# Optimization experiments

Measured on AMD Instinct MI355X. Metric: run time of the kernel, lower is better.

The kernel has to match this reference:

```python
import jax, jax.numpy as jnp
import numpy as np

HEAD, DIM, R = 8, 256, 3
RA = (2 * R + 1) ** 2  # 49


def conv2d(x, w, b=None, pad=0, groups=1):
    y = jax.lax.conv_general_dilated(x, w, (1, 1), [(pad, pad), (pad, pad)],
                                     dimension_numbers=('NCHW', 'OIHW', 'NCHW'),
                                     feature_group_count=groups)
    return y if b is None else y + b[None, :, None, None]


def grid_sample(img, grid, mode, padding='zeros'):
    # img [B,C,H,W]; grid [B,Hg,Wg,2] with (x,y) in [-1,1]; align_corners=False.
    B, C, H, W = img.shape
    Hg, Wg = grid.shape[1], grid.shape[2]
    gx = ((grid[..., 0] + 1.0) * W - 1.0) / 2.0
    gy = ((grid[..., 1] + 1.0) * H - 1.0) / 2.0
    if padding == 'border':
        gx = jnp.clip(gx, 0.0, W - 1.0)
        gy = jnp.clip(gy, 0.0, H - 1.0)
    gx = gx.reshape(B, -1)
    gy = gy.reshape(B, -1)

    def gather(iy, ix):
        iyc = jnp.clip(iy, 0, H - 1)
        ixc = jnp.clip(ix, 0, W - 1)
        return jax.vmap(lambda im, a, b: im[:, a, b])(img, iyc, ixc)  # [B,C,N]

    def mask(iy, ix):
        if padding == 'border':
            return jnp.ones(iy.shape, img.dtype)
        return ((ix >= 0) & (ix < W) & (iy >= 0) & (iy < H)).astype(img.dtype)

    if mode == 'nearest':
        ix = jnp.round(gx).astype(jnp.int32)
        iy = jnp.round(gy).astype(jnp.int32)
        out = gather(iy, ix) * mask(iy, ix)[:, None, :]
    else:  # bilinear
        x0f = jnp.floor(gx); y0f = jnp.floor(gy)
        wx = gx - x0f; wy = gy - y0f
        x0 = x0f.astype(jnp.int32); y0 = y0f.astype(jnp.int32)
        out = jnp.zeros((B, C, gx.shape[1]), img.dtype)
        for dx, dy, w in ((0, 0, (1 - wx) * (1 - wy)), (1, 0, wx * (1 - wy)),
                          (0, 1, (1 - wx) * wy), (1, 1, wx * wy)):
            ix = x0 + dx; iy = y0 + dy
            out = out + gather(iy, ix) * (w * mask(iy, ix))[:, None, :]
    return out.reshape(B, C, Hg, Wg)


def mlp2(x, W1, b1, W2, b2):
    return jax.nn.relu(x @ W1.T + b1) @ W2.T + b2


def setup_inputs() -> dict:
    key = jax.random.key(0)
    ks = jax.random.split(key, 32)
    B, H, W, Q = 1, 64, 64, 4096
    f32 = jnp.float32
    rn = lambda k, shp, s=0.02: jax.random.normal(k, shp, f32) * s
    return {
        'inp': jax.random.normal(ks[0], (B, 3, H, W), f32),
        'coord': jax.random.uniform(ks[1], (B, Q, 2), f32, -1.0, 1.0),
        'cell': jnp.full((B, Q, 2), 2.0 / (2 * H), f32),
        'W_enc': rn(ks[2], (64, 3, 3, 3)), 'b_enc': jnp.zeros((64,), f32),
        'W_ch': rn(ks[3], (256, 64, 3, 3)), 'b_ch': jnp.zeros((256,), f32),
        'W_q': rn(ks[4], (256, 256, 3, 3)), 'b_q': jnp.zeros((256,), f32),
        'W_k': rn(ks[5], (256, 256, 3, 3)), 'b_k': jnp.zeros((256,), f32),
        'W_v': rn(ks[6], (256, 256, 3, 3)), 'b_v': jnp.zeros((256,), f32),
        'W_off1': rn(ks[7], (256, 32, 5, 5)), 'b_off1': jnp.zeros((256,), f32),
        'ln_g': jnp.ones((256,), f32), 'ln_b': jnp.zeros((256,), f32),
        'W_off2': rn(ks[8], (98, 256, 1, 1)),
        'Wc1': rn(ks[9], (256, 98)), 'bc1': jnp.zeros((256,), f32),
        'Wc2': rn(ks[10], (49, 256)), 'bc2': jnp.zeros((49,), f32),
        'Wi1': rn(ks[11], (256, 12546)), 'bi1': jnp.zeros((256,), f32),
        'Wi2': rn(ks[12], (3, 256)), 'bi2': jnp.zeros((3,), f32),
        'scale': 2,
    }


def reference(inp, coord, cell, W_enc, b_enc, W_ch, b_ch, W_q, b_q, W_k, b_k,
              W_v, b_v, W_off1, b_off1, ln_g, ln_b, W_off2, Wc1, bc1, Wc2, bc2,
              Wi1, bi1, Wi2, bi2, scale):
    B, _, H, W = inp.shape
    Q = coord.shape[1]
    # gen_feat: encoder stub (conv+relu) -> conv_ch -> q/k/v convs
    feat = conv2d(jax.nn.relu(conv2d(inp, W_enc, b_enc, pad=1)), W_ch, b_ch, pad=1)
    fq = conv2d(feat, W_q, b_q, pad=1)
    fk = conv2d(feat, W_k, b_k, pad=1)
    fv = conv2d(feat, W_v, b_v, pad=1)
    # offset branch: grouped 5x5 conv -> channelwise LN -> GELU -> 1x1 conv (no bias)
    o = conv2d(feat, W_off1, b_off1, pad=2, groups=8)
    oc = o.transpose(0, 2, 3, 1)
    mu = oc.mean(-1, keepdims=True)
    var = ((oc - mu) ** 2).mean(-1, keepdims=True)
    oc = (oc - mu) / jnp.sqrt(var + 1e-5) * ln_g + ln_b
    offsets = conv2d(jax.nn.gelu(oc.transpose(0, 3, 1, 2), approximate=False), W_off2, None, pad=0)  # [B,98,H,W]
    # LR coordinate grid (y,x) at pixel centers in [-1,1]
    ys = -1.0 + 1.0 / H + (2.0 / H) * jnp.arange(H, dtype=inp.dtype)
    xs = -1.0 + 1.0 / W + (2.0 / W) * jnp.arange(W, dtype=inp.dtype)
    coord_lr = jnp.broadcast_to(jnp.stack(jnp.meshgrid(ys, xs, indexing='ij'), 0)[None], (B, 2, H, W))
    sc = coord[:, :, None, :]          # [B,Q,1,2] (y,x)
    g = sc[..., ::-1]                  # (x,y) for grid_sample
    sck = grid_sample(coord_lr, g, 'nearest').transpose(0, 2, 3, 1)  # [B,Q,1,2]
    off = grid_sample(offsets, g, 'nearest').transpose(0, 2, 3, 1).reshape(B, Q, RA, 2)
    off = jnp.tanh(off) * jnp.array([1.0 / (H - 1.0), 1.0 / (W - 1.0)], inp.dtype) * 2.0
    d = jnp.linspace(-R, R, 2 * R + 1).astype(inp.dtype)
    delta = jnp.stack(jnp.meshgrid(d * (2.0 / H), d * (2.0 / W), indexing='ij'), -1).reshape(1, 1, RA, 2)
    sck = sck + delta + off            # [B,Q,49,2] sampling locs (y,x)
    q = grid_sample(fq, g, 'bilinear').transpose(0, 2, 3, 1).reshape(B, Q, HEAD, DIM // HEAD)
    k = grid_sample(fk, sck[..., ::-1], 'nearest').transpose(0, 2, 3, 1).reshape(B, Q, RA, HEAD, DIM // HEAD)
    v = grid_sample(fv, sck[..., ::-1], 'nearest').transpose(0, 2, 3, 1).reshape(B, Q, RA, HEAD, DIM // HEAD)
    attn_val = jnp.einsum('bqhd,bqkhd->bqkh', q, k) / np.sqrt(DIM // HEAD)  # [B,Q,49,8]
    rel = (sc - sck) * jnp.array([H, W], inp.dtype)  # [B,Q,49,2]
    wcoord = mlp2(rel.reshape(B * Q, RA * 2), Wc1, bc1, Wc2, bc2).reshape(B, Q, RA, 1)
    attn = jax.nn.softmax(wcoord + attn_val, axis=2)  # softmax over 49 samples
    feat_in = (v * attn[..., None]).reshape(B, Q, RA * DIM)
    rel_cell = cell * jnp.array([H, W], inp.dtype)
    feat_in = jnp.concatenate([feat_in, rel_cell], -1)  # [B,Q,12546]
    pred = mlp2(feat_in.reshape(B * Q, -1), Wi1, bi1, Wi2, bi2).reshape(B, Q, 3)
    skip = grid_sample(inp, g, 'bilinear', 'border')[:, :, :, 0].transpose(0, 2, 1)
    return pred + skip
```

## Files before the change

### kernel.cpp

```cpp
#include <hip/hip_runtime.h>
#include <hip/hip_bf16.h>


typedef unsigned short u16;
typedef unsigned int u32;
using frag_ab = __attribute__((ext_vector_type(8))) short;
using frag_cd = __attribute__((ext_vector_type(4))) float;

#define HW 4096
#define NQ 4096
#define KBIG 12576
#define SPLITK 16
#define KCHUNK 800
#define KQ 2304
#define QSPLIT 2
#define QCHUNK 1152

static __device__ __forceinline__ u16 f2b(float f) {
  union { __hip_bfloat16 h; u16 u; } c; c.h = __float2bfloat16(f); return c.u;
}
static __device__ __forceinline__ float b2f(u16 v) {
  return __uint_as_float((u32)v << 16);
}
static __device__ __forceinline__ u32 pk2(float a, float b) {
  union { __hip_bfloat162 h; u32 u; } c;
  c.h = __float22bfloat162_rn(float2{a, b});
  return c.u;
}
static __device__ __forceinline__ void glds16(const u16* g, u16* l) {
  __builtin_amdgcn_global_load_lds(
      (const __attribute__((address_space(1))) u32*)(g),
      (__attribute__((address_space(3))) u32*)(l), 16, 0, 0);
}

#define BM 64
#define BN 64
#define BK 32
#define LDSS 40

__global__ __launch_bounds__(256)
void gemm_bt(const u16* __restrict__ A, const u16* __restrict__ Bt,
             void* __restrict__ Cv, const float* __restrict__ bias,
             int N, int K, int ldc, int flags,
             long sA, long sB, long sC, int sBias)
{
  __shared__ u16 As[BM * LDSS];
  __shared__ u16 Bs[BN * LDSS];
  const int z = blockIdx.z;
  A  += (long)z * sA;
  Bt += (long)z * sB;
  const float* bz = bias ? bias + (long)z * sBias : nullptr;

  const int tid  = threadIdx.x;
  const int m0   = blockIdx.x * BM;
  const int n0   = blockIdx.y * BN;
  const int wave = tid >> 6, lane = tid & 63;
  const int mw = (wave & 1) * 32, nw = (wave >> 1) * 32;
  const int lr = lane & 15, lk = lane >> 4;
  const int srow = tid >> 2, scol = (tid & 3) * 8;

  frag_cd acc[2][2] = {};
  const u16* aptr = A + (size_t)(m0 + srow) * K + scol;
  const bool bok  = (n0 + srow) < N;
  const u16* bptr = Bt + (size_t)(n0 + srow) * K + scol;

  uint4 av = *(const uint4*)(aptr);
  uint4 bv = bok ? *(const uint4*)(bptr) : uint4{0u, 0u, 0u, 0u};

  for (int k0 = 0; k0 < K; k0 += BK) {
    *(uint4*)&As[srow * LDSS + scol] = av;
    *(uint4*)&Bs[srow * LDSS + scol] = bv;
    __syncthreads();
    if (k0 + BK < K) {
      av = *(const uint4*)(aptr + k0 + BK);
      bv = bok ? *(const uint4*)(bptr + k0 + BK) : uint4{0u, 0u, 0u, 0u};
    }
    frag_ab af0 = *(const frag_ab*)&As[(mw      + lr) * LDSS + lk * 8];
    frag_ab af1 = *(const frag_ab*)&As[(mw + 16 + lr) * LDSS + lk * 8];
    frag_ab bf0 = *(const frag_ab*)&Bs[(nw      + lr) * LDSS + lk * 8];
    frag_ab bf1 = *(const frag_ab*)&Bs[(nw + 16 + lr) * LDSS + lk * 8];
    acc[0][0] = __builtin_amdgcn_mfma_f32_16x16x32_bf16(af0, bf0, acc[0][0], 0, 0, 0);
    acc[0][1] = __builtin_amdgcn_mfma_f32_16x16x32_bf16(af0, bf1, acc[0][1], 0, 0, 0);
    acc[1][0] = __builtin_amdgcn_mfma_f32_16x16x32_bf16(af1, bf0, acc[1][0], 0, 0, 0);
    acc[1][1] = __builtin_amdgcn_mfma_f32_16x16x32_bf16(af1, bf1, acc[1][1], 0, 0, 0);
    __syncthreads();
  }

  const bool relu = flags & 1;
  const bool obf  = flags & 2;
  #pragma unroll
  for (int i = 0; i < 2; i++)
    #pragma unroll
    for (int j = 0; j < 2; j++) {
      int col = n0 + nw + j * 16 + lr;
      if (col >= N) continue;
      float badd = bz ? bz[col] : 0.f;
      #pragma unroll
      for (int r = 0; r < 4; r++) {
        int row = m0 + mw + i * 16 + lk * 4 + r;
        float v = acc[i][j][r] + badd;
        if (relu) v = fmaxf(v, 0.f);
        size_t idx = (size_t)z * sC + (size_t)row * ldc + col;
        if (obf) ((u16*)Cv)[idx] = f2b(v);
        else     ((float*)Cv)[idx] = v;
      }
    }
}

template<int W3, int SH, int PAD>
__global__ __launch_bounds__(256)
void gemm_conv(const u16* __restrict__ feat, const u16* __restrict__ Bt,
               void* __restrict__ Cv, const float* __restrict__ bias,
               int N, int K, int ldc, int flags, int FC, int cbStride,
               long sB, long sC, int sBias)
{
  __shared__ u16 As[BM * LDSS];
  __shared__ u16 Bs[BN * LDSS];
  const int z = blockIdx.z;
  Bt += (long)z * sB;
  const float* bz = bias ? bias + (long)z * sBias : nullptr;
  const int cb = z * cbStride;

  const int tid  = threadIdx.x;
  const int m0   = blockIdx.x * BM;
  const int n0   = blockIdx.y * BN;
  const int wave = tid >> 6, lane = tid & 63;
  const int mw = (wave & 1) * 32, nw = (wave >> 1) * 32;
  const int lr = lane & 15, lk = lane >> 4;
  const int srow = tid >> 2, scol = (tid & 3) * 8;
  const int p = m0 + srow, y = p >> 6, x = p & 63;

  frag_cd acc[2][2] = {};
  const bool bok  = (n0 + srow) < N;
  const u16* bptr = Bt + (size_t)(n0 + srow) * K + scol;

  auto stageA = [&](int k0) -> uint4 {
    int k = k0 + scol;
    int s = k >> SH;
    int c = k & ((1 << SH) - 1);
    int dy = s / W3, dx = s - dy * W3;
    int yy = y + dy - PAD, xx = x + dx - PAD;
    if (((unsigned)yy < 64u) && ((unsigned)xx < 64u))
      return *(const uint4*)&feat[(size_t)(yy * 64 + xx) * FC + cb + c];
    return uint4{0u, 0u, 0u, 0u};
  };

  uint4 av = stageA(0);
  uint4 bv = bok ? *(const uint4*)(bptr) : uint4{0u, 0u, 0u, 0u};

  for (int k0 = 0; k0 < K; k0 += BK) {
    *(uint4*)&As[srow * LDSS + scol] = av;
    *(uint4*)&Bs[srow * LDSS + scol] = bv;
    __syncthreads();
    if (k0 + BK < K) {
      av = stageA(k0 + BK);
      bv = bok ? *(const uint4*)(bptr + k0 + BK) : uint4{0u, 0u, 0u, 0u};
    }
    frag_ab af0 = *(const frag_ab*)&As[(mw      + lr) * LDSS + lk * 8];
    frag_ab af1 = *(const frag_ab*)&As[(mw + 16 + lr) * LDSS + lk * 8];
    frag_ab bf0 = *(const frag_ab*)&Bs[(nw      + lr) * LDSS + lk * 8];
    frag_ab bf1 = *(const frag_ab*)&Bs[(nw + 16 + lr) * LDSS + lk * 8];
    acc[0][0] = __builtin_amdgcn_mfma_f32_16x16x32_bf16(af0, bf0, acc[0][0], 0, 0, 0);
    acc[0][1] = __builtin_amdgcn_mfma_f32_16x16x32_bf16(af0, bf1, acc[0][1], 0, 0, 0);
    acc[1][0] = __builtin_amdgcn_mfma_f32_16x16x32_bf16(af1, bf0, acc[1][0], 0, 0, 0);
    acc[1][1] = __builtin_amdgcn_mfma_f32_16x16x32_bf16(af1, bf1, acc[1][1], 0, 0, 0);
    __syncthreads();
  }

  const bool relu = flags & 1;
  const bool obf  = flags & 2;
  #pragma unroll
  for (int i = 0; i < 2; i++)
    #pragma unroll
    for (int j = 0; j < 2; j++) {
      int col = n0 + nw + j * 16 + lr;
      if (col >= N) continue;
      float badd = bz ? bz[col] : 0.f;
      #pragma unroll
      for (int r = 0; r < 4; r++) {
        int row = m0 + mw + i * 16 + lk * 4 + r;
        float v = acc[i][j][r] + badd;
        if (relu) v = fmaxf(v, 0.f);
        size_t idx = (size_t)z * sC + (size_t)row * ldc + col;
        if (obf) ((u16*)Cv)[idx] = f2b(v);
        else     ((float*)Cv)[idx] = v;
      }
    }
}

__global__ __launch_bounds__(256)
void gemm_qkv(const u16* __restrict__ feat, const u16* __restrict__ Bt,
              u16* __restrict__ P)
{
  __shared__ u16 As[64 * LDSS];
  __shared__ u16 Bs[128 * 32];
  const int tid  = threadIdx.x;
  const int m0   = blockIdx.x * 64;
  const int n0   = blockIdx.y * 128;
  const int z    = blockIdx.z;
  const int kbeg = z * QCHUNK;
  const int kend = kbeg + QCHUNK;
  const int wave = tid >> 6, lane = tid & 63;
  const int nw = wave * 32;
  const int lr = lane & 15, lk = lane >> 4;
  const int arow = tid >> 2, acol = (tid & 3) * 8;
  const int p = m0 + arow, y = p >> 6, x = p & 63;

  frag_cd acc[4][2] = {};
  const u16* bbase = Bt + (size_t)(n0 + (tid >> 2)) * KQ + (tid & 3) * 8 + kbeg;
  u16* bdst = &Bs[(size_t)tid * 8];

  auto stageA = [&](int k0) -> uint4 {
    int k = k0 + acol;
    int s = k >> 8, c = k & 255;
    int dy = s / 3, dx = s - dy * 3;
    int yy = y + dy - 1, xx = x + dx - 1;
    if (((unsigned)yy < 64u) && ((unsigned)xx < 64u))
      return *(const uint4*)&feat[(size_t)(yy * 64 + xx) * 256 + c];
    return uint4{0u, 0u, 0u, 0u};
  };

  uint4 av = stageA(kbeg);

  for (int k0 = kbeg; k0 < kend; k0 += BK) {
    glds16(bbase + (k0 - kbeg), bdst);
    glds16(bbase + (k0 - kbeg) + (size_t)64 * KQ, bdst + 2048);
    *(uint4*)&As[arow * LDSS + acol] = av;
    __syncthreads();
    if (k0 + BK < kend) av = stageA(k0 + BK);
    frag_ab af[4];
    #pragma unroll
    for (int i = 0; i < 4; i++)
      af[i] = *(const frag_ab*)&As[(i * 16 + lr) * LDSS + lk * 8];
    #pragma unroll
    for (int j = 0; j < 2; j++) {
      frag_ab bf = *(const frag_ab*)&Bs[(nw + j * 16 + lr) * 32 + lk * 8];
      #pragma unroll
      for (int i = 0; i < 4; i++)
        acc[i][j] = __builtin_amdgcn_mfma_f32_16x16x32_bf16(af[i], bf, acc[i][j], 0, 0, 0);
    }
    __syncthreads();
  }

  #pragma unroll
  for (int i = 0; i < 4; i++)
    #pragma unroll
    for (int j = 0; j < 2; j++) {
      int col = n0 + nw + j * 16 + lr;
      #pragma unroll
      for (int r = 0; r < 4; r++) {
        int row = m0 + i * 16 + lk * 4 + r;
        P[(size_t)z * (NQ * 768) + (size_t)row * 768 + col] = f2b(acc[i][j][r]);
      }
    }
}

__global__ __launch_bounds__(256)
void reduce_qkv(const u16* __restrict__ P, const float* __restrict__ bias,
                u16* __restrict__ outb, float* __restrict__ outV)
{
  int i8 = blockIdx.x * 256 + threadIdx.x;
  if (i8 >= NQ * 96) return;
  size_t i = (size_t)i8 * 8;
  int row = (int)(i / 768);
  int c = (int)(i % 768);
  uint4 a = *(const uint4*)&P[i];
  uint4 b = *(const uint4*)&P[(size_t)NQ * 768 + i];
  u32 aw[4] = {a.x, a.y, a.z, a.w};
  u32 bw[4] = {b.x, b.y, b.z, b.w};
  float v[8];
  #pragma unroll
  for (int t = 0; t < 4; t++) {
    v[2 * t]     = __uint_as_float(aw[t] << 16) + __uint_as_float(bw[t] << 16)
                 + bias[c + 2 * t];
    v[2 * t + 1] = __uint_as_float(aw[t] & 0xffff0000u)
                 + __uint_as_float(bw[t] & 0xffff0000u) + bias[c + 2 * t + 1];
  }
  uint4 ob = {pk2(v[0], v[1]), pk2(v[2], v[3]), pk2(v[4], v[5]), pk2(v[6], v[7])};
  *(uint4*)&outb[i] = ob;
  if (c >= 512) {
    float* dst = outV + (size_t)row * 256 + (c - 512);
    *(float4*)dst       = float4{v[0], v[1], v[2], v[3]};
    *(float4*)(dst + 4) = float4{v[4], v[5], v[6], v[7]};
  }
}

__global__ __launch_bounds__(512, 4)
void gemm_big(const u16* __restrict__ Bt, const float* __restrict__ fqkvV,
              const float* __restrict__ attnval, const int* __restrict__ vidx,
              const float* __restrict__ cell, u16* __restrict__ P)
{
  __shared__ u16 As[128 * LDSS];
  __shared__ u16 Bs[256 * 32];
  __shared__ int   s_vidx[5 * 128];
  __shared__ float s_attn[5 * 128 * 8];
  const int tid  = threadIdx.x;
  const int m0   = blockIdx.x * 128;
  const int z    = blockIdx.y;
  const int kbeg = z * KCHUNK;
  const int kend = min(KBIG, kbeg + KCHUNK);
  const int jbeg = kbeg >> 8;
  const int jcnt = ((kend - 1) >> 8) - jbeg + 1;
  const int wave = tid >> 6, lane = tid & 63;
  const int mw = (wave & 1) * 64, nwv = (wave >> 1) * 64;
  const int lr = lane & 15, lk = lane >> 4;
  const int arow = tid >> 2, acol = (tid & 3) * 8;
  const int q = m0 + arow;

  for (int t = tid; t < 128 * jcnt; t += 512) {
    int r = t & 127, jj = t >> 7;
    int j = jbeg + jj;
    s_vidx[t] = (j < 49) ? vidx[(m0 + r) * 49 + j] : -1;
  }
  for (int t = tid; t < 128 * 8 * jcnt; t += 512) {
    int h = t & 7, rr = (t >> 3) & 127, jj = t >> 10;
    int j = jbeg + jj;
    s_attn[t] = (j < 49) ? attnval[((size_t)((m0 + rr) * 49 + j)) * 8 + h] : 0.f;
  }
  __syncthreads();

  auto loadA = [&](int k0, float4& f0, float4& f1, float& w) {
    const int k = k0 + acol;
    const int j = k >> 8, c = k & 255;
    f0 = float4{0.f, 0.f, 0.f, 0.f};
    f1 = float4{0.f, 0.f, 0.f, 0.f};
    w = 0.f;
    if (j < 49) {
      const int jj = j - jbeg;
      int id = s_vidx[jj * 128 + arow];
      if (id >= 0) {
        w = s_attn[(jj * 128 + arow) * 8 + (c >> 5)];
        const float* src = fqkvV + (size_t)id * 256 + c;
        f0 = *(const float4*)src;
        f1 = *(const float4*)(src + 4);
      }
    } else if (c == 0) {
      f0.x = cell[q * 2]; f0.y = cell[q * 2 + 1];
      w = 64.f;
    }
  };

  frag_cd acc[4][4] = {};
  float4 f0c, f1c; float wc_;
  loadA(kbeg, f0c, f1c, wc_);
  const u16* bbase = Bt + (size_t)(tid >> 2) * KBIG + (tid & 3) * 8 + kbeg;
  u16* bdst = &Bs[(size_t)tid * 8];

  for (int k0 = kbeg; k0 < kend; k0 += BK) {
    glds16(bbase + (k0 - kbeg), bdst);
    glds16(bbase + (k0 - kbeg) + (size_t)128 * KBIG, bdst + 4096);
    {
      uint4 av;
      av.x = pk2(f0c.x * wc_, f0c.y * wc_);
      av.y = pk2(f0c.z * wc_, f0c.w * wc_);
      av.z = pk2(f1c.x * wc_, f1c.y * wc_);
      av.w = pk2(f1c.z * wc_, f1c.w * wc_);
      *(uint4*)&As[arow * LDSS + acol] = av;
    }
    __syncthreads();
    if (k0 + BK < kend) loadA(k0 + BK, f0c, f1c, wc_);
    frag_ab af[4];
    #pragma unroll
    for (int i = 0; i < 4; i++)
      af[i] = *(const frag_ab*)&As[(mw + i * 16 + lr) * LDSS + lk * 8];
    #pragma unroll
    for (int j = 0; j < 4; j++) {
      frag_ab bf = *(const frag_ab*)&Bs[(nwv + j * 16 + lr) * 32 + lk * 8];
      #pragma unroll
      for (int i = 0; i < 4; i++)
        acc[i][j] = __builtin_amdgcn_mfma_f32_16x16x32_bf16(af[i], bf, acc[i][j], 0, 0, 0);
    }
    __syncthreads();
  }

  #pragma unroll
  for (int i = 0; i < 4; i++)
    #pragma unroll
    for (int j = 0; j < 4; j++) {
      int col = nwv + j * 16 + lr;
      #pragma unroll
      for (int r = 0; r < 4; r++) {
        int row = m0 + mw + i * 16 + lk * 4 + r;
        P[(size_t)z * (NQ * 256) + (size_t)row * 256 + col] = f2b(acc[i][j][r]);
      }
    }
}

__global__ __launch_bounds__(256)
void reduce_final(const u16* __restrict__ Pb, const float* __restrict__ bi1,
                  const float* __restrict__ Wi2, const float* __restrict__ bi2,
                  const float* __restrict__ skipb, float* __restrict__ out)
{
  const int q = blockIdx.x, c = threadIdx.x;
  float s = 0.f;
  #pragma unroll
  for (int z = 0; z < SPLITK; z++)
    s += b2f(Pb[(size_t)z * (NQ * 256) + (size_t)q * 256 + c]);
  s += bi1[c];
  s = fmaxf(s, 0.f);

  __shared__ float part[3][4];
  float p0 = s * Wi2[c], p1 = s * Wi2[256 + c], p2 = s * Wi2[512 + c];
  #pragma unroll
  for (int off = 32; off; off >>= 1) {
    p0 += __shfl_xor(p0, off);
    p1 += __shfl_xor(p1, off);
    p2 += __shfl_xor(p2, off);
  }
  if ((c & 63) == 0) {
    int w = c >> 6;
    part[0][w] = p0; part[1][w] = p1; part[2][w] = p2;
  }
  __syncthreads();
  if (c < 3)
    out[q * 3 + c] = bi2[c] + skipb[q * 3 + c]
                   + part[c][0] + part[c][1] + part[c][2] + part[c][3];
}

static __device__ __forceinline__
void packconv(const float* __restrict__ W, u16* __restrict__ Bt,
              int Cin, int K2, int idx)
{
  int o  = idx / (Cin * K2);
  int r  = idx - o * (Cin * K2);
  int ci = r / K2;
  int s  = r - ci * K2;
  Bt[(size_t)o * (Cin * K2) + s * Cin + ci] = f2b(W[idx]);
}
static __device__ __forceinline__
void packcast(const float* __restrict__ W, u16* __restrict__ Bt,
              int Kin, int Kout, int idx)
{
  int n = idx / Kout, k = idx - n * Kout;
  Bt[idx] = f2b(k < Kin ? W[(size_t)n * Kin + k] : 0.f);
}

#define SZ_CH   147456
#define SZ_QKV  589824
#define SZ_OFF1 204800
#define SZ_OFF2 25088
#define SZ_C1   32768
#define SZ_C2   12544
#define SZ_PACK (SZ_CH + 3*SZ_QKV + SZ_OFF1 + SZ_OFF2 + SZ_C1 + SZ_C2 + 768)

__global__ void pack_misc(const float* W_ch, const float* W_q, const float* W_k,
                          const float* W_v, const float* W_off1, const float* W_off2,
                          const float* Wc1, const float* Wc2,
                          const float* b_q, const float* b_k, const float* b_v,
                          u16* Btch, u16* Btqkv, u16* Btoff1, u16* Btoff2,
                          u16* Btc1, u16* Btc2, float* bqkv)
{
  int i = blockIdx.x * 256 + threadIdx.x;
  if (i < SZ_CH) { packconv(W_ch, Btch, 64, 9, i); return; }
  i -= SZ_CH;
  if (i < SZ_QKV) { packconv(W_q, Btqkv, 256, 9, i); return; }
  i -= SZ_QKV;
  if (i < SZ_QKV) { packconv(W_k, Btqkv + (size_t)256 * 2304, 256, 9, i); return; }
  i -= SZ_QKV;
  if (i < SZ_QKV) { packconv(W_v, Btqkv + (size_t)512 * 2304, 256, 9, i); return; }
  i -= SZ_QKV;
  if (i < SZ_OFF1) { packconv(W_off1, Btoff1, 32, 25, i); return; }
  i -= SZ_OFF1;
  if (i < SZ_OFF2) { packcast(W_off2, Btoff2, 256, 256, i); return; }
  i -= SZ_OFF2;
  if (i < SZ_C1) { packcast(Wc1, Btc1, 98, 128, i); return; }
  i -= SZ_C1;
  if (i < SZ_C2) { packcast(Wc2, Btc2, 256, 256, i); return; }
  i -= SZ_C2;
  if (i < 768) {
    bqkv[i] = (i < 256) ? b_q[i] : (i < 512) ? b_k[i - 256] : b_v[i - 512];
  }
}

__global__ void pack_cast(const float* __restrict__ W, u16* __restrict__ Bt,
                          int N, int Kin, int Kout)
{
  int idx = blockIdx.x * 256 + threadIdx.x;
  if (idx >= N * Kout) return;
  int n = idx / Kout, k = idx - n * Kout;
  Bt[idx] = f2b(k < Kin ? W[(size_t)n * Kin + k] : 0.f);
}

__global__ __launch_bounds__(64)
void conv_enc(const float* __restrict__ inp, const float* __restrict__ W,
              const float* __restrict__ b, u16* __restrict__ feat1)
{
  const int p = blockIdx.x, c = threadIdx.x;
  const int y = p >> 6, x = p & 63;
  float s = b[c];
  #pragma unroll
  for (int ci = 0; ci < 3; ci++)
    #pragma unroll
    for (int dy = 0; dy < 3; dy++) {
      int yy = y + dy - 1;
      if ((unsigned)yy >= 64u) continue;
      #pragma unroll
      for (int dx = 0; dx < 3; dx++) {
        int xx = x + dx - 1;
        if ((unsigned)xx >= 64u) continue;
        s += inp[ci * HW + yy * 64 + xx] * W[((c * 3 + ci) * 3 + dy) * 3 + dx];
      }
    }
  feat1[(size_t)p * 64 + c] = f2b(fmaxf(s, 0.f));
}

__global__ __launch_bounds__(256)
void ln_gelu(const float* __restrict__ x, const float* __restrict__ g,
             const float* __restrict__ b, u16* __restrict__ y)
{
  const int p = blockIdx.x, c = threadIdx.x;
  __shared__ float r1[4], r2[4];
  float v = x[(size_t)p * 256 + c];
  float s1 = v, s2 = v * v;
  #pragma unroll
  for (int off = 32; off; off >>= 1) {
    s1 += __shfl_xor(s1, off);
    s2 += __shfl_xor(s2, off);
  }
  if ((c & 63) == 0) { r1[c >> 6] = s1; r2[c >> 6] = s2; }
  __syncthreads();
  float t1 = r1[0] + r1[1] + r1[2] + r1[3];
  float t2 = r2[0] + r2[1] + r2[2] + r2[3];
  float mu  = t1 * (1.f / 256.f);
  float var = t2 * (1.f / 256.f) - mu * mu;
  float xn = (v - mu) * rsqrtf(var + 1e-5f) * g[c] + b[c];
  float ge = 0.5f * xn * (1.f + erff(xn * 0.70710678118654752f));
  y[(size_t)p * 256 + c] = f2b(ge);
}

__global__ __launch_bounds__(256)
void sampler(const float* __restrict__ coord, const u16* __restrict__ fqkvb,
             const float* __restrict__ offs, const float* __restrict__ inp,
             float* __restrict__ attnval, u16* __restrict__ relbuf,
             int* __restrict__ vidx, float* __restrict__ skipb)
{
  const int q = blockIdx.x;
  const int tid = threadIdx.x;
  __shared__ float s_off[98];
  __shared__ int s_idx[49];
  __shared__ float s_q[256];

  const float c0 = coord[q * 2], c1 = coord[q * 2 + 1];
  const float gxp = ((c1 + 1.f) * 64.f - 1.f) * 0.5f;
  const float gyp = ((c0 + 1.f) * 64.f - 1.f) * 0.5f;
  const int ixn = (int)rintf(gxp), iyn = (int)rintf(gyp);
  const bool inn = ((unsigned)ixn < 64u) && ((unsigned)iyn < 64u);

  if (tid < 98) {
    float v = inn ? offs[(size_t)(iyn * 64 + ixn) * 98 + tid] : 0.f;
    s_off[tid] = tanhf(v) * (2.f / 63.f);
  }
  __syncthreads();

  const float scky = inn ? (-1.f + (float)(2 * iyn + 1) * (1.f / 64.f)) : 0.f;
  const float sckx = inn ? (-1.f + (float)(2 * ixn + 1) * (1.f / 64.f)) : 0.f;

  if (tid < 49) {
    const int a = tid / 7, bb = tid - a * 7;
    float sy = scky + (float)(a - 3) * (2.f / 64.f) + s_off[2 * tid];
    float sx = sckx + (float)(bb - 3) * (2.f / 64.f) + s_off[2 * tid + 1];
    relbuf[(size_t)q * 128 + 2 * tid]     = f2b((c0 - sy) * 64.f);
    relbuf[(size_t)q * 128 + 2 * tid + 1] = f2b((c1 - sx) * 64.f);
    float gx2 = ((sx + 1.f) * 64.f - 1.f) * 0.5f;
    float gy2 = ((sy + 1.f) * 64.f - 1.f) * 0.5f;
    int ix2 = (int)rintf(gx2), iy2 = (int)rintf(gy2);
    int id = (((unsigned)ix2 < 64u) && ((unsigned)iy2 < 64u)) ? (iy2 * 64 + ix2) : -1;
    s_idx[tid] = id;
    vidx[q * 49 + tid] = id;
  } else if (tid >= 98 && tid < 128) {
    relbuf[(size_t)q * 128 + tid] = 0;
  }

  {
    const float x0f = floorf(gxp), y0f = floorf(gyp);
    const float wx = gxp - x0f, wy = gyp - y0f;
    const int x0 = (int)x0f, y0 = (int)y0f;
    float qc = 0.f;
    #pragma unroll
    for (int t = 0; t < 4; t++) {
      int xi = x0 + (t & 1), yi = y0 + (t >> 1);
      if (((unsigned)xi < 64u) && ((unsigned)yi < 64u)) {
        float w = ((t & 1) ? wx : 1.f - wx) * ((t >> 1) ? wy : 1.f - wy);
        qc += w * b2f(fqkvb[(size_t)(yi * 64 + xi) * 768 + tid]);
      }
    }
    s_q[tid] = qc * 0.17677669529663687f;
  }

  if (tid < 3) {
    float gx = fminf(fmaxf(gxp, 0.f), 63.f);
    float gy = fminf(fmaxf(gyp, 0.f), 63.f);
    float xf = floorf(gx), yf = floorf(gy);
    float wxs = gx - xf, wys = gy - yf;
    int xa = (int)xf, ya = (int)yf;
    int xb = min(xa + 1, 63), yb = min(ya + 1, 63);
    const float* ch = inp + tid * HW;
    float v = (1.f - wxs) * (1.f - wys) * ch[ya * 64 + xa]
            + wxs * (1.f - wys) * ch[ya * 64 + xb]
            + (1.f - wxs) * wys * ch[yb * 64 + xa]
            + wxs * wys * ch[yb * 64 + xb];
    skipb[q * 3 + tid] = v;
  }
  __syncthreads();

  const int wave = tid >> 6, lane = tid & 63;
  const int half = lane >> 5, sub = lane & 31;
  const int ch0 = sub * 8;
  const int h = sub >> 2;
  float qv[8];
  #pragma unroll
  for (int i = 0; i < 8; i++) qv[i] = s_q[ch0 + i];

  for (int it = 0; it < 7; it++) {
    int j = it * 8 + wave * 2 + half;
    if (j >= 49) break;
    int id = s_idx[j];
    float p = 0.f;
    if (id >= 0) {
      uint4 kv = *(const uint4*)&fqkvb[(size_t)id * 768 + 256 + ch0];
      u32 w0 = kv.x, w1 = kv.y, w2 = kv.z, w3 = kv.w;
      p = fmaf(qv[0], __uint_as_float(w0 << 16), p);
      p = fmaf(qv[1], __uint_as_float(w0 & 0xffff0000u), p);
      p = fmaf(qv[2], __uint_as_float(w1 << 16), p);
      p = fmaf(qv[3], __uint_as_float(w1 & 0xffff0000u), p);
      p = fmaf(qv[4], __uint_as_float(w2 << 16), p);
      p = fmaf(qv[5], __uint_as_float(w2 & 0xffff0000u), p);
      p = fmaf(qv[6], __uint_as_float(w3 << 16), p);
      p = fmaf(qv[7], __uint_as_float(w3 & 0xffff0000u), p);
    }
    p += __shfl_down(p, 2, 4);
    p += __shfl_down(p, 1, 4);
    if ((sub & 3) == 0) attnval[((size_t)q * 49 + j) * 8 + h] = p;
  }
}

__global__ __launch_bounds__(512)
void softmax_k(const float* __restrict__ wc, float* __restrict__ attnval)
{
  const int q = blockIdx.x;
  const int tid = threadIdx.x;
  const int hh = tid >> 6, l = tid & 63;
  float v = (l < 49) ? wc[(size_t)q * 49 + l] + attnval[((size_t)q * 49 + l) * 8 + hh]
                     : -1e30f;
  float m = v;
  #pragma unroll
  for (int off = 32; off; off >>= 1) m = fmaxf(m, __shfl_xor(m, off));
  float e = (l < 49) ? expf(v - m) : 0.f;
  float s = e;
  #pragma unroll
  for (int off = 32; off; off >>= 1) s += __shfl_xor(s, off);
  if (l < 49) attnval[((size_t)q * 49 + l) * 8 + hh] = e / s;
}

extern "C" void kernel_launch(void* const* d_in, const int* in_sizes, int n_in,
                              void* d_out, int out_size, void* d_ws, size_t ws_size,
                              hipStream_t stream)
{
  const float* inp    = (const float*)d_in[0];
  const float* coord  = (const float*)d_in[1];
  const float* cell   = (const float*)d_in[2];
  const float* W_enc  = (const float*)d_in[3];
  const float* b_enc  = (const float*)d_in[4];
  const float* W_ch   = (const float*)d_in[5];
  const float* b_ch   = (const float*)d_in[6];
  const float* W_q    = (const float*)d_in[7];
  const float* b_q    = (const float*)d_in[8];
  const float* W_k    = (const float*)d_in[9];
  const float* b_k    = (const float*)d_in[10];
  const float* W_v    = (const float*)d_in[11];
  const float* b_v    = (const float*)d_in[12];
  const float* W_off1 = (const float*)d_in[13];
  const float* b_off1 = (const float*)d_in[14];
  const float* ln_g   = (const float*)d_in[15];
  const float* ln_b   = (const float*)d_in[16];
  const float* W_off2 = (const float*)d_in[17];
  const float* Wc1    = (const float*)d_in[18];
  const float* bc1    = (const float*)d_in[19];
  const float* Wc2    = (const float*)d_in[20];
  const float* bc2    = (const float*)d_in[21];
  const float* Wi1    = (const float*)d_in[22];
  const float* bi1    = (const float*)d_in[23];
  const float* Wi2    = (const float*)d_in[24];
  const float* bi2    = (const float*)d_in[25];

  char* base = (char*)d_ws;
  size_t off = 0;
  auto alloc = [&](size_t bytes) -> char* {
    char* r = base + off;
    off = (off + bytes + 255) & ~(size_t)255;
    return r;
  };

  float* obuf   = (float*)alloc((size_t)HW * 256 * 4);
  u16*   ocg    = (u16*)  alloc((size_t)HW * 256 * 2);
  float* offsb  = (float*)alloc((size_t)HW * 98 * 4);
  u16*   feat1  = (u16*)  alloc((size_t)HW * 64 * 2);
  u16*   feat   = (u16*)  alloc((size_t)HW * 256 * 2);
  u16*   hid1   = (u16*)  alloc((size_t)NQ * 256 * 2);
  float* wcb    = (float*)alloc((size_t)NQ * 49 * 4);
  u16*   relbuf = (u16*)  alloc((size_t)NQ * 128 * 2);
  u16*   Btqkv  = (u16*)  alloc((size_t)768 * 2304 * 2);
  u16*   Btch   = (u16*)  alloc((size_t)256 * 576 * 2);
  u16*   Btoff1 = (u16*)  alloc((size_t)256 * 800 * 2);
  u16*   Btoff2 = (u16*)  alloc((size_t)98 * 256 * 2);
  u16*   Btc1   = (u16*)  alloc((size_t)256 * 128 * 2);
  u16*   Btc2   = (u16*)  alloc((size_t)49 * 256 * 2);
  u16* Pb = (u16*)base;
  u16* Pqb = (u16*)(base + ((size_t)36 << 20));
  {
    size_t need = ((size_t)36 << 20) + (size_t)QSPLIT * NQ * 768 * 2;
    if (off < need) off = (need + 255) & ~(size_t)255;
  }
  u16*   fqkvb   = (u16*)  alloc((size_t)HW * 768 * 2);
  float* fqkvV   = (float*)alloc((size_t)HW * 256 * 4);
  float* attnval = (float*)alloc((size_t)NQ * 49 * 8 * 4);
  int*   vidxb   = (int*)  alloc((size_t)NQ * 49 * 4);
  float* skipb   = (float*)alloc((size_t)NQ * 3 * 4);
  u16*   Wi1p    = (u16*)  alloc((size_t)256 * KBIG * 2);
  float* bqkv    = (float*)alloc(768 * 4);
  (void)ws_size; (void)in_sizes; (void)n_in; (void)out_size;

  pack_misc<<<(SZ_PACK + 255) / 256, 256, 0, stream>>>(
      W_ch, W_q, W_k, W_v, W_off1, W_off2, Wc1, Wc2, b_q, b_k, b_v,
      Btch, Btqkv, Btoff1, Btoff2, Btc1, Btc2, bqkv);
  pack_cast<<<(256 * KBIG + 255) / 256, 256, 0, stream>>>(Wi1, Wi1p, 256, 12546, KBIG);

  conv_enc<<<HW, 64, 0, stream>>>(inp, W_enc, b_enc, feat1);
  gemm_conv<3, 6, 1><<<dim3(64, 4, 1), 256, 0, stream>>>(
      feat1, Btch, feat, b_ch, 256, 576, 256, 2, 64, 0, 0, 0, 0);
  gemm_qkv<<<dim3(64, 6, QSPLIT), 256, 0, stream>>>(feat, Btqkv, Pqb);
  reduce_qkv<<<(NQ * 96 + 255) / 256, 256, 0, stream>>>(Pqb, bqkv, fqkvb, fqkvV);
  gemm_conv<5, 5, 2><<<dim3(64, 1, 8), 256, 0, stream>>>(
      feat, Btoff1, obuf, b_off1, 32, 800, 256, 0, 256, 32,
      (long)32 * 800, 32, 32);
  ln_gelu<<<HW, 256, 0, stream>>>(obuf, ln_g, ln_b, ocg);
  gemm_bt<<<dim3(64, 2, 1), 256, 0, stream>>>(ocg, Btoff2, offsb, nullptr,
      98, 256, 98, 0, 0, 0, 0, 0);

  sampler<<<NQ, 256, 0, stream>>>(coord, fqkvb, offsb, inp,
                                  attnval, relbuf, vidxb, skipb);
  gemm_bt<<<dim3(64, 4, 1), 256, 0, stream>>>(relbuf, Btc1, hid1, bc1,
      256, 128, 256, 3, 0, 0, 0, 0);
  gemm_bt<<<dim3(64, 1, 1), 256, 0, stream>>>(hid1, Btc2, wcb, bc2,
      49, 256, 49, 0, 0, 0, 0, 0);
  softmax_k<<<NQ, 512, 0, stream>>>(wcb, attnval);

  gemm_big<<<dim3(32, SPLITK), 512, 0, stream>>>(
      Wi1p, fqkvV, attnval, vidxb, cell, Pb);
  reduce_final<<<NQ, 256, 0, stream>>>(Pb, bi1, Wi2, bi2, skipb, (float*)d_out);
}
```

Before: 293.9 us.

## Fuse coordinate MLP and softmax into one kernel, merge weight packing, split QKV three ways

Replaces the two small coordinate-MLP GEMM launches and the softmax kernel with a single coord_mlp kernel. It keeps the hidden layer in LDS, converts Wc2 to bf16 on the fly and applies softmax per query/head in place on attnval. This drops launches and global round trips, but runs only 64 blocks and uses a serial per-thread softmax over 49 strided global loads. The Wi1 cast is folded into the main pack kernel, and the QKV split-K goes from 2 to 3 with a generalized reduce.

New measurement: 326.9 us. 11.2% more time.

```diff
diff --git a/kernel.cpp b/kernel.cpp
--- a/kernel.cpp
+++ b/kernel.cpp
@@ -13,8 +13,8 @@
 #define SPLITK 16
 #define KCHUNK 800
 #define KQ 2304
-#define QSPLIT 2
-#define QCHUNK 1152
+#define QSPLIT 3
+#define QCHUNK 768
 
 static __device__ __forceinline__ u16 f2b(float f) {
   union { __hip_bfloat16 h; u16 u; } c; c.h = __float2bfloat16(f); return c.u;
@@ -264,17 +264,17 @@
   size_t i = (size_t)i8 * 8;
   int row = (int)(i / 768);
   int c = (int)(i % 768);
-  uint4 a = *(const uint4*)&P[i];
-  uint4 b = *(const uint4*)&P[(size_t)NQ * 768 + i];
-  u32 aw[4] = {a.x, a.y, a.z, a.w};
-  u32 bw[4] = {b.x, b.y, b.z, b.w};
   float v[8];
   #pragma unroll
-  for (int t = 0; t < 4; t++) {
-    v[2 * t]     = __uint_as_float(aw[t] << 16) + __uint_as_float(bw[t] << 16)
-                 + bias[c + 2 * t];
-    v[2 * t + 1] = __uint_as_float(aw[t] & 0xffff0000u)
-                 + __uint_as_float(bw[t] & 0xffff0000u) + bias[c + 2 * t + 1];
+  for (int t = 0; t < 8; t++) v[t] = bias[c + t];
+  for (int z = 0; z < QSPLIT; z++) {
+    uint4 a = *(const uint4*)&P[(size_t)z * (NQ * 768) + i];
+    u32 aw[4] = {a.x, a.y, a.z, a.w};
+    #pragma unroll
+    for (int t = 0; t < 4; t++) {
+      v[2 * t]     += __uint_as_float(aw[t] << 16);
+      v[2 * t + 1] += __uint_as_float(aw[t] & 0xffff0000u);
+    }
   }
   uint4 ob = {pk2(v[0], v[1]), pk2(v[2], v[3]), pk2(v[4], v[5]), pk2(v[6], v[7])};
   *(uint4*)&outb[i] = ob;
@@ -417,6 +417,117 @@
                    + part[c][0] + part[c][1] + part[c][2] + part[c][3];
 }
 
+__global__ __launch_bounds__(256)
+void coord_mlp(const u16* __restrict__ relbuf, const u16* __restrict__ Btc1,
+               const float* __restrict__ bc1, const float* __restrict__ Wc2,
+               const float* __restrict__ bc2, float* __restrict__ attnval)
+{
+  __shared__ u16 smem[25600];
+  u16*   s_rel = smem;
+  u16*   s_hid = smem + 64 * 136;
+  float* s_log = (float*)smem;
+  const int tid  = threadIdx.x;
+  const int m0   = blockIdx.x * 64;
+  const int wave = tid >> 6, lane = tid & 63;
+  const int lr = lane & 15, lk = lane >> 4;
+
+  #pragma unroll
+  for (int e = 0; e < 2; e++) {
+    int lin = tid + e * 256;
+    int row = lin >> 4, c8 = (lin & 15) * 8;
+    *(uint4*)&s_rel[row * 136 + c8] =
+        *(const uint4*)&relbuf[(size_t)(m0 + row) * 128 + c8];
+  }
+  __syncthreads();
+
+  {
+    frag_cd acc[4][4] = {};
+    const int nw = wave * 64;
+    for (int kk = 0; kk < 4; kk++) {
+      frag_ab af[4];
+      #pragma unroll
+      for (int i = 0; i < 4; i++)
+        af[i] = *(const frag_ab*)&s_rel[(i * 16 + lr) * 136 + kk * 32 + lk * 8];
+      #pragma unroll
+      for (int t = 0; t < 4; t++) {
+        int n = nw + t * 16 + lr;
+        frag_ab bf = *(const frag_ab*)&Btc1[(size_t)n * 128 + kk * 32 + lk * 8];
+        #pragma unroll
+        for (int i = 0; i < 4; i++)
+          acc[i][t] = __builtin_amdgcn_mfma_f32_16x16x32_bf16(af[i], bf, acc[i][t], 0, 0, 0);
+      }
+    }
+    #pragma unroll
+    for (int i = 0; i < 4; i++)
+      #pragma unroll
+      for (int t = 0; t < 4; t++) {
+        int col = nw + t * 16 + lr;
+        float badd = bc1[col];
+        #pragma unroll
+        for (int r = 0; r < 4; r++) {
+          int row = i * 16 + lk * 4 + r;
+          s_hid[row * 264 + col] = f2b(fmaxf(acc[i][t][r] + badd, 0.f));
+        }
+      }
+  }
+  __syncthreads();
+
+  {
+    frag_cd acc[4] = {};
+    const int nt = wave * 16;
+    const int n = nt + lr;
+    for (int kk = 0; kk < 8; kk++) {
+      frag_ab bf;
+      if (n < 49) {
+        const float* wp = Wc2 + (size_t)n * 256 + kk * 32 + lk * 8;
+        float4 w0 = *(const float4*)wp;
+        float4 w1 = *(const float4*)(wp + 4);
+        union { u16 s[8]; frag_ab f; } u;
+        u.s[0] = f2b(w0.x); u.s[1] = f2b(w0.y); u.s[2] = f2b(w0.z); u.s[3] = f2b(w0.w);
+        u.s[4] = f2b(w1.x); u.s[5] = f2b(w1.y); u.s[6] = f2b(w1.z); u.s[7] = f2b(w1.w);
+        bf = u.f;
+      } else {
+        bf = frag_ab{0, 0, 0, 0, 0, 0, 0, 0};
+      }
+      #pragma unroll
+      for (int i = 0; i < 4; i++) {
+        frag_ab af = *(const frag_ab*)&s_hid[(i * 16 + lr) * 264 + kk * 32 + lk * 8];
+        acc[i] = __builtin_amdgcn_mfma_f32_16x16x32_bf16(af, bf, acc[i], 0, 0, 0);
+      }
+    }
+    const int col = nt + lr;
+    const float badd = (col < 49) ? bc2[col] : 0.f;
+    #pragma unroll
+    for (int i = 0; i < 4; i++)
+      #pragma unroll
+      for (int r = 0; r < 4; r++) {
+        int row = i * 16 + lk * 4 + r;
+        s_log[row * 64 + col] = acc[i][r] + badd;
+      }
+  }
+  __syncthreads();
+
+  for (int p = tid; p < 512; p += 256) {
+    int ql = p >> 3, h = p & 7;
+    const size_t base = ((size_t)(m0 + ql) * 49) * 8 + h;
+    float m = -1e30f;
+    for (int j = 0; j < 49; j++) {
+      float v = s_log[ql * 64 + j] + attnval[base + (size_t)j * 8];
+      m = fmaxf(m, v);
+    }
+    float sum = 0.f;
+    for (int j = 0; j < 49; j++) {
+      float v = s_log[ql * 64 + j] + attnval[base + (size_t)j * 8];
+      sum += expf(v - m);
+    }
+    float inv = 1.f / sum;
+    for (int j = 0; j < 49; j++) {
+      float v = s_log[ql * 64 + j] + attnval[base + (size_t)j * 8];
+      attnval[base + (size_t)j * 8] = expf(v - m) * inv;
+    }
+  }
+}
+
 static __device__ __forceinline__
 void packconv(const float* __restrict__ W, u16* __restrict__ Bt,
               int Cin, int K2, int idx)
@@ -440,15 +551,15 @@
 #define SZ_OFF1 204800
 #define SZ_OFF2 25088
 #define SZ_C1   32768
-#define SZ_C2   12544
-#define SZ_PACK (SZ_CH + 3*SZ_QKV + SZ_OFF1 + SZ_OFF2 + SZ_C1 + SZ_C2 + 768)
-
-__global__ void pack_misc(const float* W_ch, const float* W_q, const float* W_k,
-                          const float* W_v, const float* W_off1, const float* W_off2,
-                          const float* Wc1, const float* Wc2,
-                          const float* b_q, const float* b_k, const float* b_v,
-                          u16* Btch, u16* Btqkv, u16* Btoff1, u16* Btoff2,
-                          u16* Btc1, u16* Btc2, float* bqkv)
+#define SZ_WI1  3219456
+#define SZ_PACK (SZ_CH + 3*SZ_QKV + SZ_OFF1 + SZ_OFF2 + SZ_C1 + 768 + SZ_WI1)
+
+__global__ void pack_all(const float* W_ch, const float* W_q, const float* W_k,
+                         const float* W_v, const float* W_off1, const float* W_off2,
+                         const float* Wc1, const float* Wi1,
+                         const float* b_q, const float* b_k, const float* b_v,
+                         u16* Btch, u16* Btqkv, u16* Btoff1, u16* Btoff2,
+                         u16* Btc1, u16* Wi1p, float* bqkv)
 {
   int i = blockIdx.x * 256 + threadIdx.x;
   if (i < SZ_CH) { packconv(W_ch, Btch, 64, 9, i); return; }
@@ -465,20 +576,12 @@
   i -= SZ_OFF2;
   if (i < SZ_C1) { packcast(Wc1, Btc1, 98, 128, i); return; }
   i -= SZ_C1;
-  if (i < SZ_C2) { packcast(Wc2, Btc2, 256, 256, i); return; }
-  i -= SZ_C2;
   if (i < 768) {
     bqkv[i] = (i < 256) ? b_q[i] : (i < 512) ? b_k[i - 256] : b_v[i - 512];
-  }
-}
-
-__global__ void pack_cast(const float* __restrict__ W, u16* __restrict__ Bt,
-                          int N, int Kin, int Kout)
-{
-  int idx = blockIdx.x * 256 + threadIdx.x;
-  if (idx >= N * Kout) return;
-  int n = idx / Kout, k = idx - n * Kout;
-  Bt[idx] = f2b(k < Kin ? W[(size_t)n * Kin + k] : 0.f);
+    return;
+  }
+  i -= 768;
+  if (i < SZ_WI1) { packcast(Wi1, Wi1p, 12546, 12576, i); }
 }
 
 __global__ __launch_bounds__(64)
@@ -632,24 +735,6 @@
     p += __shfl_down(p, 1, 4);
     if ((sub & 3) == 0) attnval[((size_t)q * 49 + j) * 8 + h] = p;
   }
-}
-
-__global__ __launch_bounds__(512)
-void softmax_k(const float* __restrict__ wc, float* __restrict__ attnval)
-{
-  const int q = blockIdx.x;
-  const int tid = threadIdx.x;
-  const int hh = tid >> 6, l = tid & 63;
-  float v = (l < 49) ? wc[(size_t)q * 49 + l] + attnval[((size_t)q * 49 + l) * 8 + hh]
-                     : -1e30f;
-  float m = v;
-  #pragma unroll
-  for (int off = 32; off; off >>= 1) m = fmaxf(m, __shfl_xor(m, off));
-  float e = (l < 49) ? expf(v - m) : 0.f;
-  float s = e;
-  #pragma unroll
-  for (int off = 32; off; off >>= 1) s += __shfl_xor(s, off);
-  if (l < 49) attnval[((size_t)q * 49 + l) * 8 + hh] = e / s;
 }
 
 extern "C" void kernel_launch(void* const* d_in, const int* in_sizes, int n_in,
@@ -696,15 +781,12 @@
   float* offsb  = (float*)alloc((size_t)HW * 98 * 4);
   u16*   feat1  = (u16*)  alloc((size_t)HW * 64 * 2);
   u16*   feat   = (u16*)  alloc((size_t)HW * 256 * 2);
-  u16*   hid1   = (u16*)  alloc((size_t)NQ * 256 * 2);
-  float* wcb    = (float*)alloc((size_t)NQ * 49 * 4);
   u16*   relbuf = (u16*)  alloc((size_t)NQ * 128 * 2);
   u16*   Btqkv  = (u16*)  alloc((size_t)768 * 2304 * 2);
   u16*   Btch   = (u16*)  alloc((size_t)256 * 576 * 2);
   u16*   Btoff1 = (u16*)  alloc((size_t)256 * 800 * 2);
   u16*   Btoff2 = (u16*)  alloc((size_t)98 * 256 * 2);
   u16*   Btc1   = (u16*)  alloc((size_t)256 * 128 * 2);
-  u16*   Btc2   = (u16*)  alloc((size_t)49 * 256 * 2);
   u16* Pb = (u16*)base;
   u16* Pqb = (u16*)(base + ((size_t)36 << 20));
   {
@@ -720,10 +802,9 @@
   float* bqkv    = (float*)alloc(768 * 4);
   (void)ws_size; (void)in_sizes; (void)n_in; (void)out_size;
 
-  pack_misc<<<(SZ_PACK + 255) / 256, 256, 0, stream>>>(
-      W_ch, W_q, W_k, W_v, W_off1, W_off2, Wc1, Wc2, b_q, b_k, b_v,
-      Btch, Btqkv, Btoff1, Btoff2, Btc1, Btc2, bqkv);
-  pack_cast<<<(256 * KBIG + 255) / 256, 256, 0, stream>>>(Wi1, Wi1p, 256, 12546, KBIG);
+  pack_all<<<(SZ_PACK + 255) / 256, 256, 0, stream>>>(
+      W_ch, W_q, W_k, W_v, W_off1, W_off2, Wc1, Wi1, b_q, b_k, b_v,
+      Btch, Btqkv, Btoff1, Btoff2, Btc1, Wi1p, bqkv);
 
   conv_enc<<<HW, 64, 0, stream>>>(inp, W_enc, b_enc, feat1);
   gemm_conv<3, 6, 1><<<dim3(64, 4, 1), 256, 0, stream>>>(
@@ -739,11 +820,7 @@
 
   sampler<<<NQ, 256, 0, stream>>>(coord, fqkvb, offsb, inp,
                                   attnval, relbuf, vidxb, skipb);
-  gemm_bt<<<dim3(64, 4, 1), 256, 0, stream>>>(relbuf, Btc1, hid1, bc1,
-      256, 128, 256, 3, 0, 0, 0, 0);
-  gemm_bt<<<dim3(64, 1, 1), 256, 0, stream>>>(hid1, Btc2, wcb, bc2,
-      49, 256, 49, 0, 0, 0, 0, 0);
-  softmax_k<<<NQ, 512, 0, stream>>>(wcb, attnval);
+  coord_mlp<<<64, 256, 0, stream>>>(relbuf, Btc1, bc1, Wc2, bc2, attnval);
 
   gemm_big<<<dim3(32, SPLITK), 512, 0, stream>>>(
       Wi1p, fqkvV, attnval, vidxb, cell, Pb);
```
